# Optimization experiments

Hardware: AMD Instinct MI355X
Metric: run time of the kernel (lower is better)

The kernel has to match this reference:

```python
import jax, jax.numpy as jnp
import numpy as np

N = 50000
E = 500000
R = 8
IN_DIM = 128
HID = 128
OUT = 128
NUM_GRAPHS = 64
EPS_BN = 1e-5


def _glorot(key, shape):
    fan_in, fan_out = shape[-2], shape[-1]
    lim = np.sqrt(6.0 / (fan_in + fan_out))
    return jax.random.uniform(key, shape, jnp.float32, -lim, lim)


def setup_inputs() -> dict:
    key = jax.random.key(0)
    ks = jax.random.split(key, 24)
    x = jax.random.normal(ks[0], (N, IN_DIM), jnp.float32)
    edge_index = jax.random.randint(ks[1], (2, E), 0, N, jnp.int64)
    edge_type = jax.random.randint(ks[2], (E,), 0, R, jnp.int64)
    batch = jnp.sort(jax.random.randint(ks[3], (N,), 0, NUM_GRAPHS, jnp.int64))
    d = {
        "x": x, "edge_index": edge_index, "edge_type": edge_type, "batch": batch,
        # RGCN layer 1 (in->hid): per-relation weights, root weight, bias
        "W1": _glorot(ks[4], (R, IN_DIM, HID)), "root1": _glorot(ks[5], (IN_DIM, HID)), "b1": jnp.zeros((HID,), jnp.float32),
        "W2": _glorot(ks[6], (R, HID, HID)), "root2": _glorot(ks[7], (HID, HID)), "b2": jnp.zeros((HID,), jnp.float32),
        "W3": _glorot(ks[8], (R, HID, HID)), "root3": _glorot(ks[9], (HID, HID)), "b3": jnp.zeros((HID,), jnp.float32),
        # BatchNorm affine params
        "g1": jnp.ones((HID,), jnp.float32), "beta1": jnp.zeros((HID,), jnp.float32),
        "g2": jnp.ones((HID,), jnp.float32), "beta2": jnp.zeros((HID,), jnp.float32),
        # attention MLP: hid -> hid//2 -> 1
        "A1": _glorot(ks[10], (HID, HID // 2)), "a1": jnp.zeros((HID // 2,), jnp.float32),
        "A2": _glorot(ks[11], (HID // 2, 1)), "a2": jnp.zeros((1,), jnp.float32),
        # combiner MLP: 2*hid -> hid -> out
        "C1": _glorot(ks[12], (2 * HID, HID)), "c1": jnp.zeros((HID,), jnp.float32),
        "C2": _glorot(ks[13], (HID, OUT)), "c2": jnp.zeros((OUT,), jnp.float32),
    }
    return d


def rgcn_conv(h, src, dst, etype, W, root, bias):
    # relation-wise gather -> mean-aggregate per (dst, relation) -> transform
    seg = dst * R + etype                                   # [E]
    msg = h[src]                                            # [E, d_in] gather
    agg = jax.ops.segment_sum(msg, seg, num_segments=N * R) # [N*R, d_in]
    cnt = jax.ops.segment_sum(jnp.ones((seg.shape[0],), h.dtype), seg, num_segments=N * R)
    agg = agg / jnp.maximum(cnt, 1.0)[:, None]              # mean aggregation (PyG default)
    agg = agg.reshape(N, R, -1)
    out = jnp.einsum('nri,rio->no', agg, W) + h @ root + bias
    return out


def batch_norm(h, gamma, beta):
    mu = jnp.mean(h, axis=0, keepdims=True)
    var = jnp.mean((h - mu) ** 2, axis=0, keepdims=True)
    return (h - mu) * jax.lax.rsqrt(var + EPS_BN) * gamma + beta


def lrelu(h):
    return jax.nn.leaky_relu(h, 0.1)


def reference(x, edge_index, edge_type, batch, W1, root1, b1, W2, root2, b2,
              W3, root3, b3, g1, beta1, g2, beta2, A1, a1, A2, a2, C1, c1, C2, c2):
    src, dst = edge_index[0], edge_index[1]
    h = rgcn_conv(x, src, dst, edge_type, W1, root1, b1)
    h = lrelu(batch_norm(h, g1, beta1))
    h = rgcn_conv(h, src, dst, edge_type, W2, root2, b2)
    h = lrelu(batch_norm(h, g2, beta2))
    node_emb = rgcn_conv(h, src, dst, edge_type, W3, root3, b3)  # [N, HID]

    # attention pooling: scores softmax-ed over ALL nodes (dim=0, as in source)
    scores = lrelu(node_emb @ A1 + a1) @ A2 + a2                 # [N, 1]
    attn = jax.nn.softmax(scores, axis=0)                        # [N, 1]
    global_emb = jax.ops.segment_sum(node_emb * attn, batch, num_segments=NUM_GRAPHS)

    combined = jnp.concatenate([node_emb, global_emb[batch]], axis=1)  # [N, 2*HID]
    final = lrelu(combined @ C1 + c1) @ C2 + c2                  # [N, OUT]
    norm = jnp.linalg.norm(final, axis=1, keepdims=True)
    return final / jnp.maximum(norm, 1e-12)
```

## Files before the change

kernel.cpp:

```cpp
#include <hip/hip_runtime.h>
#include <hip/hip_bf16.h>

typedef unsigned int u32;
typedef unsigned short u16;
typedef __bf16 bf16_t;
typedef bf16_t bf16x8 __attribute__((ext_vector_type(8)));
typedef float f32x4 __attribute__((ext_vector_type(4)));

constexpr int NN = 50000;
constexpr int EE = 500000;
constexpr int RR = 8;
constexpr int NKEY = RR * NN;
constexpr int PAIR_B = (NKEY + 511) / 512;

constexpr int WX_A1T = 0;
constexpr int WX_C1T = 8192;
constexpr int WX_C2T = 40960;
constexpr int WX_A2  = 57344;
constexpr int WX_a1  = 57408;
constexpr int WX_c1  = 57472;
constexpr int WX_c2  = 57600;
constexpr int WX_a2s = 57728;
constexpr int WX_TOT = 57729;

__device__ __forceinline__ float bf2f(u32 v){
  union { u32 u; float f; } x; x.u = (v & 0xFFFFu) << 16; return x.f;
}
__device__ __forceinline__ u16 f2bf(float f){
  union { u32 u; float f; } x; x.f = f;
  u32 r = x.u + 0x7FFFu + ((x.u >> 16) & 1u);
  return (u16)(r >> 16);
}
__device__ __forceinline__ float lrelu(float x){ return x > 0.f ? x : 0.1f * x; }
__device__ __forceinline__ float ldf(const void* p, int i, u32 fm){
  return fm ? ((const float*)p)[i] : bf2f(((const u16*)p)[i]);
}
__device__ __forceinline__ void gl_lds16(const u16* g, u16* l){
  __builtin_amdgcn_global_load_lds((const __attribute__((address_space(1))) u32*)g,
                                   (__attribute__((address_space(3))) u32*)l, 16, 0, 0);
}
__device__ __forceinline__ bf16x8 cvt8(float4 a, float4 b){
  union { bf16x8 v; u16 s[8]; } r;
  r.s[0]=f2bf(a.x); r.s[1]=f2bf(a.y); r.s[2]=f2bf(a.z); r.s[3]=f2bf(a.w);
  r.s[4]=f2bf(b.x); r.s[5]=f2bf(b.y); r.s[6]=f2bf(b.z); r.s[7]=f2bf(b.w);
  return r.v;
}

__global__ void k_fdetect(const void* x, u32* md){
  __shared__ u32 c;
  if (threadIdx.x == 0) c = 0;
  __syncthreads();
  const u16* p = (const u16*)x;
  u32 loc = 0;
  for (int j = 0; j < 16; j++){
    u16 v = p[threadIdx.x * 16 + j];
    u32 e = (v >> 7) & 0xFF;
    if (e >= 0xFD) loc++;
  }
  atomicAdd(&c, loc);
  __syncthreads();
  if (threadIdx.x == 0) md[0] = (c >= 4) ? 1u : 0u;
}
__global__ void k_idetect(const void* et, u32* md){
  __shared__ u32 c;
  if (threadIdx.x == 0) c = 0;
  __syncthreads();
  const int* p = (const int*)et;
  u32 loc = 0;
  for (int j = 0; j < 8; j++){
    int idx = 2 * (threadIdx.x * 8 + j) + 1;
    if (p[idx] != 0) loc++;
  }
  atomicAdd(&c, loc);
  __syncthreads();
  if (threadIdx.x == 0) md[1] = (c == 0) ? 1u : 0u;
}

__global__ void k_icvt(const void* ei, const void* et, const void* bat,
                       int* ei_c, int* et_c, int* bat_c, u32* __restrict__ cnt,
                       const u32* md){
  u32 im = md[1];
  int i = blockIdx.x * 256 + threadIdx.x;
  if (i < EE){
    const int* p = (const int*)ei;
    ei_c[i] = im ? p[2 * i] : p[i];
  } else if (i < 2 * EE){
    int j = i - EE;
    const int* p = (const int*)ei;
    const int* pt = (const int*)et;
    int d = im ? p[2 * i] : p[i];
    int r = im ? pt[2 * j] : pt[j];
    ei_c[i] = d;
    atomicAdd(&cnt[d * RR + r], 1u);
  } else if (i < 3 * EE){
    int j = i - 2 * EE;
    const int* p = (const int*)et;
    et_c[j] = im ? p[2 * j] : p[j];
  } else if (i < 3 * EE + NN){
    int j = i - 3 * EE;
    const int* p = (const int*)bat;
    bat_c[j] = im ? p[2 * j] : p[j];
  }
}

__global__ void k_xcvt(const void* x, u16* xb, const u32* md, u32* flags){
  u32 fm = md[0];
  int i4 = (blockIdx.x * 256 + threadIdx.x) * 4;
  if (i4 >= NN * 128) return;
  float v[4];
  if (fm){
    float4 f = *(const float4*)((const float*)x + i4);
    v[0]=f.x; v[1]=f.y; v[2]=f.z; v[3]=f.w;
  } else {
    uint2 u = *(const uint2*)((const u16*)x + i4);
    v[0]=bf2f(u.x); v[1]=bf2f(u.x>>16); v[2]=bf2f(u.y); v[3]=bf2f(u.y>>16);
  }
  bool bad = false;
  u16 o[4];
  for (int j = 0; j < 4; j++){
    if (v[j] != v[j]){ bad = true; v[j] = 0.f; }
    o[j] = f2bf(v[j]);
  }
  unsigned long long bal = __ballot(bad);
  if (bal && (threadIdx.x & 63) == 0) atomicOr(flags, 2u);
  uint2 st;
  st.x = (u32)o[0] | ((u32)o[1] << 16);
  st.y = (u32)o[2] | ((u32)o[3] << 16);
  *(uint2*)(xb + i4) = st;
}

__global__ void k_wcat(const void* W1, const void* r1, const void* W2, const void* r2,
                       const void* W3, const void* r3, u16* wcatT, const u32* md, u32* flags){
  u32 fm = md[0];
  int idx = blockIdx.x * 256 + threadIdx.x;
  if (idx >= 3 * 128 * 1152) return;
  int L = idx / (128 * 1152);
  int rem = idx % (128 * 1152);
  int n = rem / 1152, k = rem % 1152;
  const void* W  = (L == 0) ? W1 : ((L == 1) ? W2 : W3);
  const void* rt = (L == 0) ? r1 : ((L == 1) ? r2 : r3);
  float v;
  if (k < 1024){
    int r = k & 7, c = k >> 3;
    v = ldf(W, (r * 128 + c) * 128 + n, fm);
  } else {
    v = ldf(rt, (k - 1024) * 128 + n, fm);
  }
  if (v != v){ v = 0.f; atomicOr(flags, 2u); }
  wcatT[idx] = f2bf(v);
}

__global__ void k_wext(const void* A1, const void* a1, const void* A2, const void* a2,
                       const void* C1, const void* c1, const void* C2, const void* c2,
                       u16* wext, const u32* md){
  u32 fm = md[0];
  int idx = blockIdx.x * 256 + threadIdx.x;
  if (idx >= WX_TOT) return;
  float v;
  if (idx < WX_C1T){
    int n = idx >> 7, k = idx & 127;
    v = ldf(A1, k * 64 + n, fm);
  } else if (idx < WX_C2T){
    int j = idx - WX_C1T; int n = j >> 8, k = j & 255;
    v = ldf(C1, k * 128 + n, fm);
  } else if (idx < WX_A2){
    int j = idx - WX_C2T; int n = j >> 7, k = j & 127;
    v = ldf(C2, k * 128 + n, fm);
  } else if (idx < WX_a1){ v = ldf(A2, idx - WX_A2, fm); }
  else if (idx < WX_c1){ v = ldf(a1, idx - WX_a1, fm); }
  else if (idx < WX_c2){ v = ldf(c1, idx - WX_c1, fm); }
  else if (idx < WX_a2s){ v = ldf(c2, idx - WX_c2, fm); }
  else { v = ldf(a2, 0, fm); }
  wext[idx] = f2bf(v);
}

__global__ void k_pairA(const u32* __restrict__ cnt, u32* __restrict__ blockSum){
  __shared__ u32 sd[256];
  int b = blockIdx.x, t = threadIdx.x;
  u32 s = 0;
  for (int j = 0; j < 2; j++){
    int key = b * 512 + t * 2 + j;
    if (key < NKEY) s += cnt[key];
  }
  sd[t] = s; __syncthreads();
  for (int off = 128; off; off >>= 1){ if (t < off) sd[t] += sd[t + off]; __syncthreads(); }
  if (t == 0) blockSum[b] = sd[0];
}
__global__ void k_pairB(const u32* __restrict__ blockSum, u32* __restrict__ blockBase){
  int lane = threadIdx.x;
  u32 loc[13]; u32 s = 0;
  for (int j = 0; j < 13; j++){
    int b = lane * 13 + j;
    u32 v = (b < PAIR_B) ? blockSum[b] : 0u;
    loc[j] = s; s += v;
  }
  u32 tot = s;
  for (int off = 1; off < 64; off <<= 1){
    u32 x = __shfl_up(tot, off);
    if (lane >= off) tot += x;
  }
  u32 excl = tot - s;
  for (int j = 0; j < 13; j++){
    int b = lane * 13 + j;
    if (b < PAIR_B) blockBase[b] = excl + loc[j];
  }
}
__global__ void k_pairC(const u32* __restrict__ cnt, const u32* __restrict__ blockBase,
                        u32* __restrict__ pairStart, u32* __restrict__ cursor){
  __shared__ u32 sd[256];
  int b = blockIdx.x, t = threadIdx.x;
  int k0 = b * 512 + t * 2;
  u32 v0 = 0, v1 = 0;
  if (k0 < NKEY) v0 = cnt[k0];
  if (k0 + 1 < NKEY) v1 = cnt[k0 + 1];
  sd[t] = v0 + v1; __syncthreads();
  for (int off = 1; off < 256; off <<= 1){
    u32 x = (t >= off) ? sd[t - off] : 0u;
    __syncthreads();
    sd[t] += x;
    __syncthreads();
  }
  u32 excl = sd[t] - (v0 + v1);
  u32 base = blockBase[b] + excl;
  if (k0 < NKEY){ pairStart[k0] = base; cursor[k0] = 0u; }
  if (k0 + 1 < NKEY){ pairStart[k0 + 1] = base + v0; cursor[k0 + 1] = 0u; }
  if (k0 + 1 == NKEY - 1) pairStart[NKEY] = base + v0 + v1;
}
__global__ void k_sort3(const int* __restrict__ ei, const int* __restrict__ et,
                        const u32* __restrict__ pairStart, u32* __restrict__ cursor,
                        u32* __restrict__ src_s){
  int e = blockIdx.x * 256 + threadIdx.x;
  if (e >= EE) return;
  int r = et[e], d = ei[EE + e];
  u32 key = (u32)d * RR + (u32)r;
  u32 p = pairStart[key] + atomicAdd(&cursor[key], 1u);
  src_s[p] = (u32)ei[e];
}

__global__ __launch_bounds__(256) void k_agg(const u16* __restrict__ h,
                                             const u32* __restrict__ pairStart,
                                             const u32* __restrict__ src_s,
                                             u16* __restrict__ agg){
  int d = blockIdx.x * 4 + (threadIdx.x >> 6);
  if (d >= NN) return;
  int lane = threadIdx.x & 63;
  const uint4* p4 = (const uint4*)(pairStart + d * 8);
  uint4 q0 = p4[0], q1 = p4[1];
  u32 ps[9];
  ps[0]=q0.x; ps[1]=q0.y; ps[2]=q0.z; ps[3]=q0.w;
  ps[4]=q1.x; ps[5]=q1.y; ps[6]=q1.z; ps[7]=q1.w;
  ps[8]=pairStart[d * 8 + 8];
  u32 jb = ps[0], je = ps[8];
  u32 pre = 0;
  if (jb + lane < je) pre = src_s[jb + lane];
  const u16* hb = h + lane * 2;
  u32 ou[8] = {0,0,0,0,0,0,0,0};
  #pragma unroll
  for (int r = 0; r < 8; r++){
    u32 s = ps[r], e = ps[r + 1];
    float a0 = 0.f, a1 = 0.f, b0 = 0.f, b1 = 0.f;
    u32 j = s;
    for (; j + 1 < e; j += 2){
      u32 i0 = j - jb;
      u32 s0 = (i0 < 64) ? __shfl(pre, (int)i0) : src_s[j];
      u32 s1 = (i0 + 1 < 64) ? __shfl(pre, (int)(i0 + 1)) : src_s[j + 1];
      u32 v0 = *(const u32*)(hb + (size_t)s0 * 128);
      u32 v1 = *(const u32*)(hb + (size_t)s1 * 128);
      a0 += bf2f(v0); a1 += bf2f(v0 >> 16);
      b0 += bf2f(v1); b1 += bf2f(v1 >> 16);
    }
    if (j < e){
      u32 i0 = j - jb;
      u32 s0 = (i0 < 64) ? __shfl(pre, (int)i0) : src_s[j];
      u32 v0 = *(const u32*)(hb + (size_t)s0 * 128);
      a0 += bf2f(v0); a1 += bf2f(v0 >> 16);
    }
    a0 += b0; a1 += b1;
    int c = (int)(e - s);
    float sc = 1.0f / (float)max(c, 1);
    u32 m0 = (u32)f2bf(a0 * sc), m1 = (u32)f2bf(a1 * sc);
    ou[r >> 1]       |= m0 << ((r & 1) * 16);
    ou[4 + (r >> 1)] |= m1 << ((r & 1) * 16);
  }
  uint4* dst = (uint4*)(agg + (size_t)d * 1024 + lane * 16);
  dst[0] = make_uint4(ou[0], ou[1], ou[2], ou[3]);
  dst[1] = make_uint4(ou[4], ou[5], ou[6], ou[7]);
}

__global__ __launch_bounds__(256) void k_gemm_big(const u16* __restrict__ h,
                                                  const u16* __restrict__ agg,
                                                  const u16* __restrict__ wT,
                                                  const void* __restrict__ bias,
                                                  float* __restrict__ out, const u32* md,
                                                  float* __restrict__ stats, int do_stats){
  __shared__ u16 As[64][64];
  __shared__ u16 Bs[64][64];
  u32 fm = md[0];
  int g = blockIdx.x;
  int mt = (g >> 4) * 8 + (g & 7);
  int nh = (g >> 3) & 1;
  int m0 = mt * 64;
  int tid = threadIdx.x;
  int w = tid >> 6, lane = tid & 63, qd = lane >> 4, l16 = lane & 15;

  int rin = lane >> 3;
  int sc8 = (lane & 7) ^ rin;

  const u16* agA[2]; const u16* hA[2]; u16* ldsA[2];
  #pragma unroll
  for (int i = 0; i < 2; i++){
    int row = (w * 2 + i) * 8 + rin;
    int node = m0 + row; if (node > NN - 1) node = NN - 1;
    agA[i] = agg + (size_t)node * 1024 + sc8 * 8;
    hA[i]  = h + (size_t)node * 128 + sc8 * 8;
    ldsA[i] = &As[(w * 2 + i) * 8][0];
  }
  const u16* wB[2]; u16* ldsB[2];
  #pragma unroll
  for (int i = 0; i < 2; i++){
    int row = (w * 2 + i) * 8 + rin;
    wB[i] = wT + (size_t)(nh * 64 + row) * 1152 + sc8 * 8;
    ldsB[i] = &Bs[(w * 2 + i) * 8][0];
  }

  f32x4 acc[4];
  #pragma unroll
  for (int j = 0; j < 4; j++) acc[j] = (f32x4){0.f,0.f,0.f,0.f};

  int sw = (l16 & 7) << 3;
  for (int k0 = 0; k0 < 1152; k0 += 64){
    __syncthreads();
    if (k0 < 1024){
      gl_lds16(agA[0] + k0, ldsA[0]);
      gl_lds16(agA[1] + k0, ldsA[1]);
    } else {
      gl_lds16(hA[0] + (k0 - 1024), ldsA[0]);
      gl_lds16(hA[1] + (k0 - 1024), ldsA[1]);
    }
    gl_lds16(wB[0] + k0, ldsB[0]);
    gl_lds16(wB[1] + k0, ldsB[1]);
    __syncthreads();
    #pragma unroll
    for (int kk = 0; kk < 64; kk += 32){
      bf16x8 a = *(const bf16x8*)(&As[w * 16 + l16][(kk + qd * 8) ^ sw]);
      #pragma unroll
      for (int ct = 0; ct < 4; ct++){
        bf16x8 b = *(const bf16x8*)(&Bs[ct * 16 + l16][(kk + qd * 8) ^ sw]);
        acc[ct] = __builtin_amdgcn_mfma_f32_16x16x32_bf16(a, b, acc[ct], 0, 0, 0);
      }
    }
  }

  float sarr[4], s2arr[4];
  #pragma unroll
  for (int ct = 0; ct < 4; ct++){
    int col = nh * 64 + ct * 16 + l16;
    float bv = ldf(bias, col, fm);
    float s = 0.f, s2 = 0.f;
    int rbase = m0 + w * 16 + qd * 4;
    #pragma unroll
    for (int rg = 0; rg < 4; rg++){
      int node = rbase + rg;
      if (node < NN){
        float v = acc[ct][rg] + bv;
        out[(size_t)node * 128 + col] = v;
        s += v; s2 += v * v;
      }
    }
    s  += __shfl_xor(s, 16);  s  += __shfl_xor(s, 32);
    s2 += __shfl_xor(s2, 16); s2 += __shfl_xor(s2, 32);
    sarr[ct] = s; s2arr[ct] = s2;
  }
  if (do_stats){
    float* red = (float*)&As[0][0];
    __syncthreads();
    if (qd == 0){
      #pragma unroll
      for (int ct = 0; ct < 4; ct++){
        red[w * 128 + ct * 16 + l16] = sarr[ct];
        red[w * 128 + 64 + ct * 16 + l16] = s2arr[ct];
      }
    }
    __syncthreads();
    if (tid < 128){
      float v = red[tid] + red[128 + tid] + red[256 + tid] + red[384 + tid];
      int which = tid >> 6, colh = tid & 63;
      unsafeAtomicAdd(&stats[which * 128 + nh * 64 + colh], v);
    }
  }
}

__global__ void k_bnapply(const float* __restrict__ out, const float* __restrict__ stats,
                          const void* __restrict__ g, const void* __restrict__ beta,
                          u16* __restrict__ hout, const u32* md, u32* flags, u32 layerbit){
  u32 fm = md[0];
  int idx = (blockIdx.x * 256 + threadIdx.x) * 4;
  if (idx >= NN * 128) return;
  int col = idx & 127;
  float4 v = *(const float4*)(out + idx);
  float vv[4] = {v.x, v.y, v.z, v.w};
  bool bad = false;
  u16 o[4];
  for (int j = 0; j < 4; j++){
    int c = col + j;
    float mu = stats[c] * (1.0f / NN);
    float var = fmaxf(stats[128 + c] * (1.0f / NN) - mu * mu, 0.f);
    float sc = ldf(g, c, fm) * rsqrtf(var + 1e-5f);
    float sh = ldf(beta, c, fm) - mu * sc;
    float r = vv[j] * sc + sh;
    if (r != r || sc != sc){ bad = true; r = 0.f; }
    o[j] = f2bf(lrelu(r));
  }
  unsigned long long bal = __ballot(bad);
  if (bal && (threadIdx.x & 63) == 0) atomicOr(flags, layerbit);
  uint2 st;
  st.x = (u32)o[0] | ((u32)o[1] << 16);
  st.y = (u32)o[2] | ((u32)o[3] << 16);
  *(uint2*)(hout + idx) = st;
}

__global__ __launch_bounds__(256) void k_scores_mfma(const float* __restrict__ emb,
                                                     const u16* __restrict__ wext,
                                                     float* __restrict__ scores, u32* smax){
  int m0 = blockIdx.x * 64;
  int tid = threadIdx.x;
  int w = tid >> 6, lane = tid & 63, qd = lane >> 4, l16 = lane & 15;
  int na = m0 + w * 16 + l16; if (na > NN - 1) na = NN - 1;
  const float* arow = emb + (size_t)na * 128;
  f32x4 acc[4];
  #pragma unroll
  for (int j = 0; j < 4; j++) acc[j] = (f32x4){0.f,0.f,0.f,0.f};
  #pragma unroll
  for (int k0 = 0; k0 < 4; k0++){
    float4 f0 = *(const float4*)(arow + k0 * 32 + qd * 8);
    float4 f1 = *(const float4*)(arow + k0 * 32 + qd * 8 + 4);
    bf16x8 a = cvt8(f0, f1);
    #pragma unroll
    for (int ct = 0; ct < 4; ct++){
      bf16x8 b = *(const bf16x8*)(wext + WX_A1T + (size_t)(ct * 16 + l16) * 128 + k0 * 32 + qd * 8);
      acc[ct] = __builtin_amdgcn_mfma_f32_16x16x32_bf16(a, b, acc[ct], 0, 0, 0);
    }
  }
  float a1v[4], a2v[4];
  #pragma unroll
  for (int ct = 0; ct < 4; ct++){
    a1v[ct] = bf2f(wext[WX_a1 + ct * 16 + l16]);
    a2v[ct] = bf2f(wext[WX_A2 + ct * 16 + l16]);
  }
  float a2s = bf2f(wext[WX_a2s]);
  float bm = -1e30f;
  #pragma unroll
  for (int rg = 0; rg < 4; rg++){
    float s = 0.f;
    #pragma unroll
    for (int ct = 0; ct < 4; ct++)
      s += lrelu(acc[ct][rg] + a1v[ct]) * a2v[ct];
    s += __shfl_xor(s, 1); s += __shfl_xor(s, 2);
    s += __shfl_xor(s, 4); s += __shfl_xor(s, 8);
    int row = m0 + w * 16 + qd * 4 + rg;
    float sf = s + a2s;
    if (row < NN){
      bm = fmaxf(bm, sf);
      if (l16 == 0) scores[row] = sf;
    }
  }
  bm = fmaxf(bm, __shfl_xor(bm, 16));
  bm = fmaxf(bm, __shfl_xor(bm, 32));
  if (lane == 0) atomicMax(smax, (bm >= -1e29f) ?
      ((__float_as_uint(bm) & 0x80000000u) ? ~__float_as_uint(bm) : (__float_as_uint(bm) | 0x80000000u)) : 0u);
}

__device__ __forceinline__ float funmap(u32 m){
  union{u32 u; float f;} x;
  x.u = (m & 0x80000000u) ? (m ^ 0x80000000u) : ~m;
  return x.f;
}

__global__ void k_expsum(const float* __restrict__ scores, const u32* smax,
                         float* __restrict__ attnw, float* ssum, u32* flags){
  float mx = funmap(*smax);
  int gid = blockIdx.x * 256 + threadIdx.x;
  if (mx != mx){ if (gid == 0) atomicOr(flags, 32u); mx = 0.f; }
  float s = 0.f;
  bool bad = false;
  for (int i = gid; i < NN; i += 256 * 128){
    float e = __expf(scores[i] - mx);
    if (e != e){ bad = true; e = 0.f; }
    attnw[i] = e; s += e;
  }
  unsigned long long bal = __ballot(bad);
  if (bal && (threadIdx.x & 63) == 0) atomicOr(flags, 32u);
  for (int off = 32; off; off >>= 1) s += __shfl_down(s, off);
  if ((threadIdx.x & 63) == 0) unsafeAtomicAdd(ssum, s);
}

constexpr int POOL_CHUNK = 32;
__global__ __launch_bounds__(128) void k_pool(const float* __restrict__ emb,
                                              const float* __restrict__ attnw,
                                              const float* __restrict__ ssum,
                                              const int* __restrict__ batch,
                                              float* __restrict__ gemb, u32* flags){
  int t = threadIdx.x;
  int n0 = blockIdx.x * POOL_CHUNK;
  if (n0 >= NN) return;
  int n1 = min(n0 + POOL_CHUNK, NN);
  float sv = *ssum;
  bool bad = !(sv > 0.f) || (sv != sv);
  if (bad && t == 0 && blockIdx.x == 0) atomicOr(flags, 64u);
  float rs = bad ? 0.f : 1.0f / sv;
  int cur = batch[n0];
  float acc = 0.f;
  for (int n = n0; n < n1; n++){
    int b = batch[n];
    if (b != cur){ unsafeAtomicAdd(&gemb[cur * 128 + t], acc * rs); acc = 0.f; cur = b; }
    acc += emb[(size_t)n * 128 + t] * attnw[n];
  }
  unsafeAtomicAdd(&gemb[cur * 128 + t], acc * rs);
}

__global__ void k_gembC(const float* __restrict__ gemb, const u16* __restrict__ wext,
                        float* __restrict__ gembC){
  int idx = blockIdx.x * 256 + threadIdx.x;
  if (idx >= 64 * 128) return;
  int g = idx >> 7, n = idx & 127;
  const float* gr = gemb + g * 128;
  const u16* wr = wext + WX_C1T + (size_t)n * 256 + 128;
  float s = 0.f;
  #pragma unroll 8
  for (int k = 0; k < 128; k++) s += gr[k] * bf2f(wr[k]);
  gembC[idx] = s + bf2f(wext[WX_c1 + n]);
}

__global__ __launch_bounds__(256) void k_final_mfma(const float* __restrict__ emb,
                                                    const float* __restrict__ gembC,
                                                    const int* __restrict__ batch,
                                                    const u16* __restrict__ wext,
                                                    void* __restrict__ outp,
                                                    const u32* md){
  __shared__ u16 Hs[64][136];
  u32 fm = md[0];
  int m0 = blockIdx.x * 64;
  int tid = threadIdx.x;
  int w = tid >> 6, lane = tid & 63, qd = lane >> 4, l16 = lane & 15;
  int na = m0 + w * 16 + l16; if (na > NN - 1) na = NN - 1;
  const float* arow = emb + (size_t)na * 128;

  f32x4 acc[8];
  #pragma unroll
  for (int j = 0; j < 8; j++) acc[j] = (f32x4){0.f,0.f,0.f,0.f};
  #pragma unroll
  for (int k0 = 0; k0 < 4; k0++){
    float4 f0 = *(const float4*)(arow + k0 * 32 + qd * 8);
    float4 f1 = *(const float4*)(arow + k0 * 32 + qd * 8 + 4);
    bf16x8 a = cvt8(f0, f1);
    #pragma unroll
    for (int ct = 0; ct < 8; ct++){
      bf16x8 b = *(const bf16x8*)(wext + WX_C1T + (size_t)(ct * 16 + l16) * 256 + k0 * 32 + qd * 8);
      acc[ct] = __builtin_amdgcn_mfma_f32_16x16x32_bf16(a, b, acc[ct], 0, 0, 0);
    }
  }
  int rbase = w * 16 + qd * 4;
  int gg[4];
  #pragma unroll
  for (int rg = 0; rg < 4; rg++){
    int node = m0 + rbase + rg; if (node > NN - 1) node = NN - 1;
    gg[rg] = batch[node];
  }
  #pragma unroll
  for (int ct = 0; ct < 8; ct++){
    int col = ct * 16 + l16;
    #pragma unroll
    for (int rg = 0; rg < 4; rg++){
      float h = acc[ct][rg] + gembC[gg[rg] * 128 + col];
      Hs[rbase + rg][col] = f2bf(lrelu(h));
    }
  }
  __syncthreads();
  f32x4 acc2[8];
  #pragma unroll
  for (int j = 0; j < 8; j++) acc2[j] = (f32x4){0.f,0.f,0.f,0.f};
  #pragma unroll
  for (int k0 = 0; k0 < 4; k0++){
    bf16x8 a = *(const bf16x8*)(&Hs[w * 16 + l16][k0 * 32 + qd * 8]);
    #pragma unroll
    for (int ct = 0; ct < 8; ct++){
      bf16x8 b = *(const bf16x8*)(wext + WX_C2T + (size_t)(ct * 16 + l16) * 128 + k0 * 32 + qd * 8);
      acc2[ct] = __builtin_amdgcn_mfma_f32_16x16x32_bf16(a, b, acc2[ct], 0, 0, 0);
    }
  }
  float c2v[8];
  #pragma unroll
  for (int ct = 0; ct < 8; ct++) c2v[ct] = bf2f(wext[WX_c2 + ct * 16 + l16]);
  #pragma unroll
  for (int rg = 0; rg < 4; rg++){
    float ss = 0.f;
    #pragma unroll
    for (int ct = 0; ct < 8; ct++){
      float o = acc2[ct][rg] + c2v[ct];
      ss += o * o;
    }
    ss += __shfl_xor(ss, 1); ss += __shfl_xor(ss, 2);
    ss += __shfl_xor(ss, 4); ss += __shfl_xor(ss, 8);
    float sc = 1.0f / fmaxf(sqrtf(ss), 1e-12f);
    int row = m0 + rbase + rg;
    if (row < NN){
      if (fm){
        float* op = (float*)outp;
        #pragma unroll
        for (int ct = 0; ct < 8; ct++)
          op[(size_t)row * 128 + ct * 16 + l16] = (acc2[ct][rg] + c2v[ct]) * sc;
      } else {
        u16* op = (u16*)outp;
        #pragma unroll
        for (int ct = 0; ct < 8; ct++)
          op[(size_t)row * 128 + ct * 16 + l16] = f2bf((acc2[ct][rg] + c2v[ct]) * sc);
      }
    }
  }
}

__global__ void k_diag(const u32* pairStart, const u32* flags, const u32* md, void* outp){
  if (threadIdx.x != 0 || blockIdx.x != 0) return;
  u32 fm = md[0];
  u32 f = flags[0];
  if (pairStart[NKEY] != (u32)EE) f |= 1u;
  for (int b = 0; b < 9; b++){
    if (f & (1u << b)){
      float s = (float)(131072 >> b);
      if (fm) ((float*)outp)[b] = s;
      else ((u16*)outp)[b] = f2bf(s);
    }
  }
}
__global__ void k_wsfail(u32* outp){ outp[0] = 0x43000000u; }

constexpr size_t O_OUT   = 0;
constexpr size_t O_H     = 25600000;
constexpr size_t O_XBF   = 38400000;
constexpr size_t O_WCAT  = 51200000;
constexpr size_t O_WEXT  = 52084736;
constexpr size_t O_EI    = 52200448;
constexpr size_t O_ET    = 56200448;
constexpr size_t O_BAT   = 58200448;
constexpr size_t O_SRC   = 58400448;
constexpr size_t O_PST   = 60400448;
constexpr size_t O_GEMBC = 62100448;
constexpr size_t O_CNT   = 62400448;
constexpr size_t O_SCO   = 65600448;
constexpr size_t O_AW    = 65800448;
constexpr size_t O_GEMB  = 66000448;
constexpr size_t O_STATS = 66033216;
constexpr size_t O_MISC  = 66035264;
constexpr size_t O_AGG   = 66035520;
constexpr size_t WS_NEED = 168435520;

extern "C" void kernel_launch(void* const* d_in, const int* in_sizes, int n_in,
                              void* d_out, int out_size, void* d_ws, size_t ws_size,
                              hipStream_t stream) {
  const void* x     = d_in[0];
  const void* ei    = d_in[1];
  const void* et    = d_in[2];
  const void* batch = d_in[3];
  const void* W1 = d_in[4],  *r1 = d_in[5],  *b1 = d_in[6];
  const void* W2 = d_in[7],  *r2 = d_in[8],  *b2 = d_in[9];
  const void* W3 = d_in[10], *r3 = d_in[11], *b3 = d_in[12];
  const void* g1 = d_in[13], *be1 = d_in[14];
  const void* g2 = d_in[15], *be2 = d_in[16];
  const void* A1 = d_in[17], *a1 = d_in[18];
  const void* A2 = d_in[19], *a2 = d_in[20];
  const void* C1 = d_in[21], *c1 = d_in[22];
  const void* C2 = d_in[23], *c2 = d_in[24];

  if (ws_size < WS_NEED){ k_wsfail<<<1, 1, 0, stream>>>((u32*)d_out); return; }
  char* ws = (char*)d_ws;
  float* out   = (float*)(ws + O_OUT);
  u16*   hbuf  = (u16*)(ws + O_H);
  u16*   xbf   = (u16*)(ws + O_XBF);
  u16*   wcat  = (u16*)(ws + O_WCAT);
  u16*   wext  = (u16*)(ws + O_WEXT);
  int*   ei_c  = (int*)(ws + O_EI);
  int*   et_c  = (int*)(ws + O_ET);
  int*   bat_c = (int*)(ws + O_BAT);
  u32*   src_s = (u32*)(ws + O_SRC);
  u32*   pairStart = (u32*)(ws + O_PST);
  float* gembC = (float*)(ws + O_GEMBC);
  u32*   cnt   = (u32*)(ws + O_CNT);
  float* sco   = (float*)(ws + O_SCO);
  float* aw    = (float*)(ws + O_AW);
  float* gemb  = (float*)(ws + O_GEMB);
  float* stats = (float*)(ws + O_STATS);
  u32*   misc  = (u32*)(ws + O_MISC);
  u16*   aggb  = (u16*)(ws + O_AGG);
  u32* cursor    = (u32*)(ws + O_OUT);
  u32* blockSum  = (u32*)(ws + O_OUT + 1600000);
  u32* blockBase = (u32*)(ws + O_OUT + 1604096);
  u32* smax = misc + 25;
  float* ssum = (float*)(misc + 26);
  u32* flags = misc + 27;
  u32* md = misc + 28;

  hipMemsetAsync(ws + O_CNT, 0, 1600000, stream);
  hipMemsetAsync(ws + O_GEMB, 0, 32768 + 2048 + 256, stream);

  k_fdetect<<<1, 256, 0, stream>>>(x, md);
  k_idetect<<<1, 256, 0, stream>>>(et, md);
  k_icvt<<<6055, 256, 0, stream>>>(ei, et, batch, ei_c, et_c, bat_c, cnt, md);
  k_xcvt<<<6250, 256, 0, stream>>>(x, xbf, md, flags);
  k_wcat<<<1728, 256, 0, stream>>>(W1, r1, W2, r2, W3, r3, wcat, md, flags);
  k_wext<<<227, 256, 0, stream>>>(A1, a1, A2, a2, C1, c1, C2, c2, wext, md);

  k_pairA<<<PAIR_B, 256, 0, stream>>>(cnt, blockSum);
  k_pairB<<<1, 64, 0, stream>>>(blockSum, blockBase);
  k_pairC<<<PAIR_B, 256, 0, stream>>>(cnt, blockBase, pairStart, cursor);
  k_sort3<<<(EE + 255) / 256, 256, 0, stream>>>(ei_c, et_c, pairStart, cursor, src_s);

  const void* bias[3] = {b1, b2, b3};
  const void* gam[2] = {g1, g2};
  const void* bet[2] = {be1, be2};
  const u16* hin = xbf;
  for (int L = 0; L < 3; L++){
    const u16* wT = wcat + (size_t)L * 128 * 1152;
    k_agg<<<(NN + 3) / 4, 256, 0, stream>>>(hin, pairStart, src_s, aggb);
    k_gemm_big<<<1568, 256, 0, stream>>>(hin, aggb, wT, bias[L], out, md,
                                         stats + (L < 2 ? L * 256 : 0), (L < 2) ? 1 : 0);
    if (L < 2){
      k_bnapply<<<6250, 256, 0, stream>>>(out, stats + L * 256, gam[L], bet[L], hbuf, md, flags, 4u << L);
      hin = hbuf;
    }
  }
  k_scores_mfma<<<(NN + 63) / 64, 256, 0, stream>>>(out, wext, sco, smax);
  k_expsum<<<128, 256, 0, stream>>>(sco, smax, aw, ssum, flags);
  k_pool<<<(NN + POOL_CHUNK - 1) / POOL_CHUNK, 128, 0, stream>>>(out, aw, ssum, bat_c, gemb, flags);
  k_gembC<<<32, 256, 0, stream>>>(gemb, wext, gembC);
  k_final_mfma<<<(NN + 63) / 64, 256, 0, stream>>>(out, gembC, bat_c, wext, d_out, md);
  k_diag<<<1, 64, 0, stream>>>(pairStart, flags, md, d_out);
}
```

Measured before the change: 618.6 us.

## Merge preprocessing launches and write bf16 embedding copy for downstream kernels

Merges the detect, convert and weight-prep kernels into fewer launches by splitting blocks on block index, and folds the diagnostic kernel into the tail of the final kernel. The last GEMM layer also writes a bf16 copy of the node embeddings into the freed x buffer, so the scores and final kernels read half the bytes and skip the fp32-to-bf16 conversion. This trims launch overhead and memory traffic, at the cost of extra bf16 stores in the last GEMM. The MFMA inner loop is split into two loops, which does not change the work done.

```diff
diff --git a/kernel.cpp b/kernel.cpp
--- a/kernel.cpp
+++ b/kernel.cpp
@@ -39,139 +39,129 @@
   __builtin_amdgcn_global_load_lds((const __attribute__((address_space(1))) u32*)g,
                                    (__attribute__((address_space(3))) u32*)l, 16, 0, 0);
 }
-__device__ __forceinline__ bf16x8 cvt8(float4 a, float4 b){
-  union { bf16x8 v; u16 s[8]; } r;
-  r.s[0]=f2bf(a.x); r.s[1]=f2bf(a.y); r.s[2]=f2bf(a.z); r.s[3]=f2bf(a.w);
-  r.s[4]=f2bf(b.x); r.s[5]=f2bf(b.y); r.s[6]=f2bf(b.z); r.s[7]=f2bf(b.w);
-  return r.v;
-}
-
-__global__ void k_fdetect(const void* x, u32* md){
+
+__global__ void k_detect(const void* x, const void* et, u32* md){
   __shared__ u32 c;
   if (threadIdx.x == 0) c = 0;
   __syncthreads();
-  const u16* p = (const u16*)x;
   u32 loc = 0;
-  for (int j = 0; j < 16; j++){
-    u16 v = p[threadIdx.x * 16 + j];
-    u32 e = (v >> 7) & 0xFF;
-    if (e >= 0xFD) loc++;
-  }
-  atomicAdd(&c, loc);
-  __syncthreads();
-  if (threadIdx.x == 0) md[0] = (c >= 4) ? 1u : 0u;
-}
-__global__ void k_idetect(const void* et, u32* md){
-  __shared__ u32 c;
-  if (threadIdx.x == 0) c = 0;
-  __syncthreads();
-  const int* p = (const int*)et;
-  u32 loc = 0;
-  for (int j = 0; j < 8; j++){
-    int idx = 2 * (threadIdx.x * 8 + j) + 1;
-    if (p[idx] != 0) loc++;
-  }
-  atomicAdd(&c, loc);
-  __syncthreads();
-  if (threadIdx.x == 0) md[1] = (c == 0) ? 1u : 0u;
-}
-
-__global__ void k_icvt(const void* ei, const void* et, const void* bat,
-                       int* ei_c, int* et_c, int* bat_c, u32* __restrict__ cnt,
-                       const u32* md){
-  u32 im = md[1];
-  int i = blockIdx.x * 256 + threadIdx.x;
-  if (i < EE){
-    const int* p = (const int*)ei;
-    ei_c[i] = im ? p[2 * i] : p[i];
-  } else if (i < 2 * EE){
-    int j = i - EE;
-    const int* p = (const int*)ei;
-    const int* pt = (const int*)et;
-    int d = im ? p[2 * i] : p[i];
-    int r = im ? pt[2 * j] : pt[j];
-    ei_c[i] = d;
-    atomicAdd(&cnt[d * RR + r], 1u);
-  } else if (i < 3 * EE){
-    int j = i - 2 * EE;
+  if (blockIdx.x == 0){
+    const u16* p = (const u16*)x;
+    for (int j = 0; j < 16; j++){
+      u16 v = p[threadIdx.x * 16 + j];
+      u32 e = (v >> 7) & 0xFF;
+      if (e >= 0xFD) loc++;
+    }
+    atomicAdd(&c, loc);
+    __syncthreads();
+    if (threadIdx.x == 0) md[0] = (c >= 4) ? 1u : 0u;
+  } else {
     const int* p = (const int*)et;
-    et_c[j] = im ? p[2 * j] : p[j];
-  } else if (i < 3 * EE + NN){
-    int j = i - 3 * EE;
-    const int* p = (const int*)bat;
-    bat_c[j] = im ? p[2 * j] : p[j];
-  }
-}
-
-__global__ void k_xcvt(const void* x, u16* xb, const u32* md, u32* flags){
+    for (int j = 0; j < 8; j++){
+      int idx = 2 * (threadIdx.x * 8 + j) + 1;
+      if (p[idx] != 0) loc++;
+    }
+    atomicAdd(&c, loc);
+    __syncthreads();
+    if (threadIdx.x == 0) md[1] = (c == 0) ? 1u : 0u;
+  }
+}
+
+__global__ void k_cvt(const void* ei, const void* et, const void* bat, const void* x,
+                      int* ei_c, int* et_c, int* bat_c, u16* xb,
+                      u32* __restrict__ cnt, const u32* md, u32* flags){
+  if (blockIdx.x < 6055){
+    u32 im = md[1];
+    int i = blockIdx.x * 256 + threadIdx.x;
+    if (i < EE){
+      const int* p = (const int*)ei;
+      ei_c[i] = im ? p[2 * i] : p[i];
+    } else if (i < 2 * EE){
+      int j = i - EE;
+      const int* p = (const int*)ei;
+      const int* pt = (const int*)et;
+      int d = im ? p[2 * i] : p[i];
+      int r = im ? pt[2 * j] : pt[j];
+      ei_c[i] = d;
+      atomicAdd(&cnt[d * RR + r], 1u);
+    } else if (i < 3 * EE){
+      int j = i - 2 * EE;
+      const int* p = (const int*)et;
+      et_c[j] = im ? p[2 * j] : p[j];
+    } else if (i < 3 * EE + NN){
+      int j = i - 3 * EE;
+      const int* p = (const int*)bat;
+      bat_c[j] = im ? p[2 * j] : p[j];
+    }
+  } else {
+    u32 fm = md[0];
+    int i4 = ((blockIdx.x - 6055) * 256 + threadIdx.x) * 4;
+    if (i4 >= NN * 128) return;
+    float v[4];
+    if (fm){
+      float4 f = *(const float4*)((const float*)x + i4);
+      v[0]=f.x; v[1]=f.y; v[2]=f.z; v[3]=f.w;
+    } else {
+      uint2 u = *(const uint2*)((const u16*)x + i4);
+      v[0]=bf2f(u.x); v[1]=bf2f(u.x>>16); v[2]=bf2f(u.y); v[3]=bf2f(u.y>>16);
+    }
+    bool bad = false;
+    u16 o[4];
+    for (int j = 0; j < 4; j++){
+      if (v[j] != v[j]){ bad = true; v[j] = 0.f; }
+      o[j] = f2bf(v[j]);
+    }
+    unsigned long long bal = __ballot(bad);
+    if (bal && (threadIdx.x & 63) == 0) atomicOr(flags, 2u);
+    uint2 st;
+    st.x = (u32)o[0] | ((u32)o[1] << 16);
+    st.y = (u32)o[2] | ((u32)o[3] << 16);
+    *(uint2*)(xb + i4) = st;
+  }
+}
+
+__global__ void k_wprep(const void* W1, const void* r1, const void* W2, const void* r2,
+                        const void* W3, const void* r3,
+                        const void* A1, const void* a1, const void* A2, const void* a2,
+                        const void* C1, const void* c1, const void* C2, const void* c2,
+                        u16* wcatT, u16* wext, const u32* md, u32* flags){
   u32 fm = md[0];
-  int i4 = (blockIdx.x * 256 + threadIdx.x) * 4;
-  if (i4 >= NN * 128) return;
-  float v[4];
-  if (fm){
-    float4 f = *(const float4*)((const float*)x + i4);
-    v[0]=f.x; v[1]=f.y; v[2]=f.z; v[3]=f.w;
+  if (blockIdx.x < 1728){
+    int idx = blockIdx.x * 256 + threadIdx.x;
+    int L = idx / (128 * 1152);
+    int rem = idx % (128 * 1152);
+    int n = rem / 1152, k = rem % 1152;
+    const void* W  = (L == 0) ? W1 : ((L == 1) ? W2 : W3);
+    const void* rt = (L == 0) ? r1 : ((L == 1) ? r2 : r3);
+    float v;
+    if (k < 1024){
+      int r = k & 7, c = k >> 3;
+      v = ldf(W, (r * 128 + c) * 128 + n, fm);
+    } else {
+      v = ldf(rt, (k - 1024) * 128 + n, fm);
+    }
+    if (v != v){ v = 0.f; atomicOr(flags, 2u); }
+    wcatT[idx] = f2bf(v);
   } else {
-    uint2 u = *(const uint2*)((const u16*)x + i4);
-    v[0]=bf2f(u.x); v[1]=bf2f(u.x>>16); v[2]=bf2f(u.y); v[3]=bf2f(u.y>>16);
-  }
-  bool bad = false;
-  u16 o[4];
-  for (int j = 0; j < 4; j++){
-    if (v[j] != v[j]){ bad = true; v[j] = 0.f; }
-    o[j] = f2bf(v[j]);
-  }
-  unsigned long long bal = __ballot(bad);
-  if (bal && (threadIdx.x & 63) == 0) atomicOr(flags, 2u);
-  uint2 st;
-  st.x = (u32)o[0] | ((u32)o[1] << 16);
-  st.y = (u32)o[2] | ((u32)o[3] << 16);
-  *(uint2*)(xb + i4) = st;
-}
-
-__global__ void k_wcat(const void* W1, const void* r1, const void* W2, const void* r2,
-                       const void* W3, const void* r3, u16* wcatT, const u32* md, u32* flags){
-  u32 fm = md[0];
-  int idx = blockIdx.x * 256 + threadIdx.x;
-  if (idx >= 3 * 128 * 1152) return;
-  int L = idx / (128 * 1152);
-  int rem = idx % (128 * 1152);
-  int n = rem / 1152, k = rem % 1152;
-  const void* W  = (L == 0) ? W1 : ((L == 1) ? W2 : W3);
-  const void* rt = (L == 0) ? r1 : ((L == 1) ? r2 : r3);
-  float v;
-  if (k < 1024){
-    int r = k & 7, c = k >> 3;
-    v = ldf(W, (r * 128 + c) * 128 + n, fm);
-  } else {
-    v = ldf(rt, (k - 1024) * 128 + n, fm);
-  }
-  if (v != v){ v = 0.f; atomicOr(flags, 2u); }
-  wcatT[idx] = f2bf(v);
-}
-
-__global__ void k_wext(const void* A1, const void* a1, const void* A2, const void* a2,
-                       const void* C1, const void* c1, const void* C2, const void* c2,
-                       u16* wext, const u32* md){
-  u32 fm = md[0];
-  int idx = blockIdx.x * 256 + threadIdx.x;
-  if (idx >= WX_TOT) return;
-  float v;
-  if (idx < WX_C1T){
-    int n = idx >> 7, k = idx & 127;
-    v = ldf(A1, k * 64 + n, fm);
-  } else if (idx < WX_C2T){
-    int j = idx - WX_C1T; int n = j >> 8, k = j & 255;
-    v = ldf(C1, k * 128 + n, fm);
-  } else if (idx < WX_A2){
-    int j = idx - WX_C2T; int n = j >> 7, k = j & 127;
-    v = ldf(C2, k * 128 + n, fm);
-  } else if (idx < WX_a1){ v = ldf(A2, idx - WX_A2, fm); }
-  else if (idx < WX_c1){ v = ldf(a1, idx - WX_a1, fm); }
-  else if (idx < WX_c2){ v = ldf(c1, idx - WX_c1, fm); }
-  else if (idx < WX_a2s){ v = ldf(c2, idx - WX_c2, fm); }
-  else { v = ldf(a2, 0, fm); }
-  wext[idx] = f2bf(v);
+    int idx = (blockIdx.x - 1728) * 256 + threadIdx.x;
+    if (idx >= WX_TOT) return;
+    float v;
+    if (idx < WX_C1T){
+      int n = idx >> 7, k = idx & 127;
+      v = ldf(A1, k * 64 + n, fm);
+    } else if (idx < WX_C2T){
+      int j = idx - WX_C1T; int n = j >> 8, k = j & 255;
+      v = ldf(C1, k * 128 + n, fm);
+    } else if (idx < WX_A2){
+      int j = idx - WX_C2T; int n = j >> 7, k = j & 127;
+      v = ldf(C2, k * 128 + n, fm);
+    } else if (idx < WX_a1){ v = ldf(A2, idx - WX_A2, fm); }
+    else if (idx < WX_c1){ v = ldf(a1, idx - WX_a1, fm); }
+    else if (idx < WX_c2){ v = ldf(c1, idx - WX_c1, fm); }
+    else if (idx < WX_a2s){ v = ldf(c2, idx - WX_c2, fm); }
+    else { v = ldf(a2, 0, fm); }
+    wext[idx] = f2bf(v);
+  }
 }
 
 __global__ void k_pairA(const u32* __restrict__ cnt, u32* __restrict__ blockSum){
@@ -292,7 +282,8 @@
                                                   const u16* __restrict__ wT,
                                                   const void* __restrict__ bias,
                                                   float* __restrict__ out, const u32* md,
-                                                  float* __restrict__ stats, int do_stats){
+                                                  float* __restrict__ stats, int do_stats,
+                                                  u16* __restrict__ embb){
   __shared__ u16 As[64][64];
   __shared__ u16 Bs[64][64];
   u32 fm = md[0];
@@ -344,7 +335,12 @@
     for (int kk = 0; kk < 64; kk += 32){
       bf16x8 a = *(const bf16x8*)(&As[w * 16 + l16][(kk + qd * 8) ^ sw]);
       #pragma unroll
-      for (int ct = 0; ct < 4; ct++){
+      for (int ct = 0; ct < 2; ct++){
+        bf16x8 b = *(const bf16x8*)(&Bs[ct * 16 + l16][(kk + qd * 8) ^ sw]);
+        acc[ct] = __builtin_amdgcn_mfma_f32_16x16x32_bf16(a, b, acc[ct], 0, 0, 0);
+      }
+      #pragma unroll
+      for (int ct = 2; ct < 4; ct++){
         bf16x8 b = *(const bf16x8*)(&Bs[ct * 16 + l16][(kk + qd * 8) ^ sw]);
         acc[ct] = __builtin_amdgcn_mfma_f32_16x16x32_bf16(a, b, acc[ct], 0, 0, 0);
       }
@@ -364,6 +360,7 @@
       if (node < NN){
         float v = acc[ct][rg] + bv;
         out[(size_t)node * 128 + col] = v;
+        if (embb) embb[(size_t)node * 128 + col] = f2bf(v);
         s += v; s2 += v * v;
       }
     }
@@ -419,22 +416,20 @@
   *(uint2*)(hout + idx) = st;
 }
 
-__global__ __launch_bounds__(256) void k_scores_mfma(const float* __restrict__ emb,
+__global__ __launch_bounds__(256) void k_scores_mfma(const u16* __restrict__ embb,
                                                      const u16* __restrict__ wext,
                                                      float* __restrict__ scores, u32* smax){
   int m0 = blockIdx.x * 64;
   int tid = threadIdx.x;
   int w = tid >> 6, lane = tid & 63, qd = lane >> 4, l16 = lane & 15;
   int na = m0 + w * 16 + l16; if (na > NN - 1) na = NN - 1;
-  const float* arow = emb + (size_t)na * 128;
+  const u16* arow = embb + (size_t)na * 128;
   f32x4 acc[4];
   #pragma unroll
   for (int j = 0; j < 4; j++) acc[j] = (f32x4){0.f,0.f,0.f,0.f};
   #pragma unroll
   for (int k0 = 0; k0 < 4; k0++){
-    float4 f0 = *(const float4*)(arow + k0 * 32 + qd * 8);
-    float4 f1 = *(const float4*)(arow + k0 * 32 + qd * 8 + 4);
-    bf16x8 a = cvt8(f0, f1);
+    bf16x8 a = *(const bf16x8*)(arow + k0 * 32 + qd * 8);
     #pragma unroll
     for (int ct = 0; ct < 4; ct++){
       bf16x8 b = *(const bf16x8*)(wext + WX_A1T + (size_t)(ct * 16 + l16) * 128 + k0 * 32 + qd * 8);
@@ -531,28 +526,28 @@
   gembC[idx] = s + bf2f(wext[WX_c1 + n]);
 }
 
-__global__ __launch_bounds__(256) void k_final_mfma(const float* __restrict__ emb,
+__global__ __launch_bounds__(256) void k_final_mfma(const u16* __restrict__ embb,
                                                     const float* __restrict__ gembC,
                                                     const int* __restrict__ batch,
                                                     const u16* __restrict__ wext,
                                                     void* __restrict__ outp,
-                                                    const u32* md){
+                                                    const u32* md,
+                                                    const u32* __restrict__ pairStart,
+                                                    const u32* __restrict__ flags){
   __shared__ u16 Hs[64][136];
   u32 fm = md[0];
   int m0 = blockIdx.x * 64;
   int tid = threadIdx.x;
   int w = tid >> 6, lane = tid & 63, qd = lane >> 4, l16 = lane & 15;
   int na = m0 + w * 16 + l16; if (na > NN - 1) na = NN - 1;
-  const float* arow = emb + (size_t)na * 128;
+  const u16* arow = embb + (size_t)na * 128;
 
   f32x4 acc[8];
   #pragma unroll
   for (int j = 0; j < 8; j++) acc[j] = (f32x4){0.f,0.f,0.f,0.f};
   #pragma unroll
   for (int k0 = 0; k0 < 4; k0++){
-    float4 f0 = *(const float4*)(arow + k0 * 32 + qd * 8);
-    float4 f1 = *(const float4*)(arow + k0 * 32 + qd * 8 + 4);
-    bf16x8 a = cvt8(f0, f1);
+    bf16x8 a = *(const bf16x8*)(arow + k0 * 32 + qd * 8);
     #pragma unroll
     for (int ct = 0; ct < 8; ct++){
       bf16x8 b = *(const bf16x8*)(wext + WX_C1T + (size_t)(ct * 16 + l16) * 256 + k0 * 32 + qd * 8);
@@ -617,21 +612,22 @@
       }
     }
   }
-}
-
-__global__ void k_diag(const u32* pairStart, const u32* flags, const u32* md, void* outp){
-  if (threadIdx.x != 0 || blockIdx.x != 0) return;
-  u32 fm = md[0];
-  u32 f = flags[0];
-  if (pairStart[NKEY] != (u32)EE) f |= 1u;
-  for (int b = 0; b < 9; b++){
-    if (f & (1u << b)){
-      float s = (float)(131072 >> b);
-      if (fm) ((float*)outp)[b] = s;
-      else ((u16*)outp)[b] = f2bf(s);
-    }
-  }
-}
+  if (blockIdx.x == 0){
+    __syncthreads();
+    if (tid == 0){
+      u32 f = flags[0];
+      if (pairStart[NKEY] != (u32)EE) f |= 1u;
+      for (int b = 0; b < 9; b++){
+        if (f & (1u << b)){
+          float s = (float)(131072 >> b);
+          if (fm) ((float*)outp)[b] = s;
+          else ((u16*)outp)[b] = f2bf(s);
+        }
+      }
+    }
+  }
+}
+
 __global__ void k_wsfail(u32* outp){ outp[0] = 0x43000000u; }
 
 constexpr size_t O_OUT   = 0;
@@ -702,12 +698,10 @@
   hipMemsetAsync(ws + O_CNT, 0, 1600000, stream);
   hipMemsetAsync(ws + O_GEMB, 0, 32768 + 2048 + 256, stream);
 
-  k_fdetect<<<1, 256, 0, stream>>>(x, md);
-  k_idetect<<<1, 256, 0, stream>>>(et, md);
-  k_icvt<<<6055, 256, 0, stream>>>(ei, et, batch, ei_c, et_c, bat_c, cnt, md);
-  k_xcvt<<<6250, 256, 0, stream>>>(x, xbf, md, flags);
-  k_wcat<<<1728, 256, 0, stream>>>(W1, r1, W2, r2, W3, r3, wcat, md, flags);
-  k_wext<<<227, 256, 0, stream>>>(A1, a1, A2, a2, C1, c1, C2, c2, wext, md);
+  k_detect<<<2, 256, 0, stream>>>(x, et, md);
+  k_cvt<<<12305, 256, 0, stream>>>(ei, et, batch, x, ei_c, et_c, bat_c, xbf, cnt, md, flags);
+  k_wprep<<<1955, 256, 0, stream>>>(W1, r1, W2, r2, W3, r3,
+                                    A1, a1, A2, a2, C1, c1, C2, c2, wcat, wext, md, flags);
 
   k_pairA<<<PAIR_B, 256, 0, stream>>>(cnt, blockSum);
   k_pairB<<<1, 64, 0, stream>>>(blockSum, blockBase);
@@ -722,16 +716,17 @@
     const u16* wT = wcat + (size_t)L * 128 * 1152;
     k_agg<<<(NN + 3) / 4, 256, 0, stream>>>(hin, pairStart, src_s, aggb);
     k_gemm_big<<<1568, 256, 0, stream>>>(hin, aggb, wT, bias[L], out, md,
-                                         stats + (L < 2 ? L * 256 : 0), (L < 2) ? 1 : 0);
+                                         stats + (L < 2 ? L * 256 : 0), (L < 2) ? 1 : 0,
+                                         (L == 2) ? xbf : (u16*)nullptr);
     if (L < 2){
       k_bnapply<<<6250, 256, 0, stream>>>(out, stats + L * 256, gam[L], bet[L], hbuf, md, flags, 4u << L);
       hin = hbuf;
     }
   }
-  k_scores_mfma<<<(NN + 63) / 64, 256, 0, stream>>>(out, wext, sco, smax);
+  k_scores_mfma<<<(NN + 63) / 64, 256, 0, stream>>>(xbf, wext, sco, smax);
   k_expsum<<<128, 256, 0, stream>>>(sco, smax, aw, ssum, flags);
   k_pool<<<(NN + POOL_CHUNK - 1) / POOL_CHUNK, 128, 0, stream>>>(out, aw, ssum, bat_c, gemb, flags);
   k_gembC<<<32, 256, 0, stream>>>(gemb, wext, gembC);
-  k_final_mfma<<<(NN + 63) / 64, 256, 0, stream>>>(out, gembC, bat_c, wext, d_out, md);
-  k_diag<<<1, 64, 0, stream>>>(pairStart, flags, md, d_out);
-}
+  k_final_mfma<<<(NN + 63) / 64, 256, 0, stream>>>(xbf, gembC, bat_c, wext, d_out, md,
+                                                   pairStart, flags);
+}
```

Result: no change. 609.7 us (-1.4%).
